# Kernel tuning notes

Hardware: AMD Instinct MI355X
Metric: run time of the kernel (lower is better)

Reference implementation:

```python
import jax, jax.numpy as jnp
import numpy as np

N_NODES = 100000
N_EDGES = 1600000
D_IN = 3      # node_hidden_dim
D_GCN = 128   # gcn_dim


def setup_inputs() -> dict:
    key = jax.random.key(0)
    ks = jax.random.split(key, 10)
    x = jax.random.normal(ks[0], (N_NODES, D_IN), dtype=jnp.float32)
    edge_index = jax.random.randint(ks[1], (2, N_EDGES), 0, N_NODES, dtype=jnp.int64)
    s_in = 1.0 / np.sqrt(D_IN)
    s_h = 1.0 / np.sqrt(D_GCN)
    # PyG SAGEConv: out = lin_l(mean_{j in N(i)} x_j) + lin_r(x_i); bias lives in lin_l
    Wl0 = jax.random.uniform(ks[2], (D_IN, D_GCN), jnp.float32, -s_in, s_in)
    Wr0 = jax.random.uniform(ks[3], (D_IN, D_GCN), jnp.float32, -s_in, s_in)
    b0 = jnp.zeros((D_GCN,), jnp.float32)
    Wl1 = jax.random.uniform(ks[4], (D_GCN, D_GCN), jnp.float32, -s_h, s_h)
    Wr1 = jax.random.uniform(ks[5], (D_GCN, D_GCN), jnp.float32, -s_h, s_h)
    b1 = jnp.zeros((D_GCN,), jnp.float32)
    ln_g = jnp.ones((D_GCN,), jnp.float32)
    ln_b = jnp.zeros((D_GCN,), jnp.float32)
    return {"x": x, "edge_index": edge_index, "Wl0": Wl0, "Wr0": Wr0, "b0": b0,
            "Wl1": Wl1, "Wr1": Wr1, "b1": b1, "ln_g": ln_g, "ln_b": ln_b}


def _sage(h, src, dst, n, inv_deg, Wl, Wr, b):
    # gather source features over edges, mean-reduce onto destinations
    agg = jax.ops.segment_sum(h[src], dst, num_segments=n) * inv_deg  # [N, d]
    return agg @ Wl + h @ Wr + b


def _layernorm(h, g, b, eps=1e-5):
    mu = jnp.mean(h, axis=-1, keepdims=True)
    var = jnp.mean(jnp.square(h - mu), axis=-1, keepdims=True)
    return (h - mu) * jax.lax.rsqrt(var + eps) * g + b


def reference(x, edge_index, Wl0, Wr0, b0, Wl1, Wr1, b1, ln_g, ln_b):
    n = x.shape[0]
    src, dst = edge_index[0], edge_index[1]
    deg = jax.ops.segment_sum(jnp.ones_like(src, dtype=x.dtype), dst, num_segments=n)
    inv_deg = (1.0 / jnp.maximum(deg, 1.0))[:, None]
    h = jax.nn.relu(_sage(x, src, dst, n, inv_deg, Wl0, Wr0, b0))  # dropout = id at eval
    h = _layernorm(h, ln_g, ln_b)
    h = jax.nn.relu(_sage(h, src, dst, n, inv_deg, Wl1, Wr1, b1))
    return h
```

## Files before the change

### kernel.cpp

```cpp
#include <hip/hip_runtime.h>


#define MD 48
#define CAPB 19968
#define MAXBIN 128
#define EPB 4096

#if defined(__has_builtin)
#if __has_builtin(__builtin_amdgcn_cvt_f32_fp8) && __has_builtin(__builtin_amdgcn_cvt_pk_fp8_f32)
#define HAVE_FP8 1
#else
#define HAVE_FP8 0
#endif
#else
#define HAVE_FP8 0
#endif

typedef __attribute__((ext_vector_type(8))) short short8;
typedef __attribute__((ext_vector_type(4))) float floatx4;

__device__ __forceinline__ unsigned bf16_rne(float f) {
    unsigned u = __float_as_uint(f);
    return (u + 0x7FFFu + ((u >> 16) & 1u)) >> 16;
}
__device__ __forceinline__ float bf_lo(unsigned u) { return __uint_as_float(u << 16); }
__device__ __forceinline__ float bf_hi(unsigned u) { return __uint_as_float(u & 0xFFFF0000u); }

__global__ __launch_bounds__(256) void k_binA(
        const int* __restrict__ src, const int* __restrict__ dst,
        int* __restrict__ bcur, unsigned* __restrict__ bins, int E, int nbin) {
    __shared__ int cnt[MAXBIN];
    __shared__ int base[MAXBIN];
    int t = threadIdx.x;
    if (t < MAXBIN) cnt[t] = 0;
    __syncthreads();

    int i0 = blockIdx.x * EPB + t * 16;
    unsigned rec[16];
    int bn[16], rk[16];
    int m = 0;
    if (i0 + 16 <= E) {
#pragma unroll
        for (int q = 0; q < 4; q++) {
            int4 d4 = *(const int4*)&dst[i0 + q * 4];
            int4 s4 = *(const int4*)&src[i0 + q * 4];
            int dd[4] = {d4.x, d4.y, d4.z, d4.w};
            int ss[4] = {s4.x, s4.y, s4.z, s4.w};
#pragma unroll
            for (int j = 0; j < 4; j++) {
                int idx = q * 4 + j;
                bn[idx] = dd[j] >> 10;
                rec[idx] = ((unsigned)(dd[j] & 1023) << 17) | (unsigned)ss[j];
                rk[idx] = atomicAdd(&cnt[bn[idx]], 1);
            }
        }
        m = 16;
    } else {
        for (int j = 0; i0 + j < E && j < 16; j++) {
            int d = dst[i0 + j], s = src[i0 + j];
            bn[j] = d >> 10;
            rec[j] = ((unsigned)(d & 1023) << 17) | (unsigned)s;
            rk[j] = atomicAdd(&cnt[bn[j]], 1);
            m++;
        }
    }
    __syncthreads();
    if (t < nbin) {
        int c = cnt[t];
        base[t] = (c > 0) ? atomicAdd(&bcur[t], c) : 0;
    }
    __syncthreads();
    for (int j = 0; j < m; j++) {
        int g = base[bn[j]] + rk[j];
        if (g < CAPB) bins[(size_t)bn[j] * CAPB + g] = rec[j];
    }
}

__global__ __launch_bounds__(256) void k_binB(
        const unsigned* __restrict__ bins, const int* __restrict__ bcur,
        int* __restrict__ counts, int* __restrict__ slots, int N) {
    __shared__ int cnt[256];
    int t = threadIdx.x;
    int bin = blockIdx.x >> 2, sub = blockIdx.x & 3;
    int llo = sub << 8;
    cnt[t] = 0;
    __syncthreads();
    int total = bcur[bin];
    if (total > CAPB) total = CAPB;
    const unsigned* brow = &bins[(size_t)bin * CAPB];
    int nbase = bin << 10;
    for (int i = t; i < total; i += 1024) {
        unsigned r0 = 0, r1 = 0, r2 = 0, r3 = 0;
        bool h0 = i < total, h1 = i + 256 < total, h2 = i + 512 < total, h3 = i + 768 < total;
        if (h0) r0 = brow[i];
        if (h1) r1 = brow[i + 256];
        if (h2) r2 = brow[i + 512];
        if (h3) r3 = brow[i + 768];
#define DEP(h, rr) if (h) { int dl = (int)(rr >> 17) - llo; \
        if ((unsigned)dl < 256u) { int r = atomicAdd(&cnt[dl], 1); \
            if (r < MD) slots[(size_t)(nbase + llo + dl) * MD + r] = (int)(rr & 0x1FFFFu); } }
        DEP(h0, r0) DEP(h1, r1) DEP(h2, r2) DEP(h3, r3)
#undef DEP
    }
    __syncthreads();
    int node = nbase + llo + t;
    if (node < N) counts[node] = cnt[t];
}

__global__ void k_pack_w(const float* __restrict__ Wl, const float* __restrict__ Wr,
                         uint4* __restrict__ Bp) {
    int g = blockIdx.x * 256 + threadIdx.x;
    int lane = g & 63, jt = (g >> 6) & 7, s = g >> 9;
    int k0 = s * 32 + ((lane >> 4) << 3);
    int n = jt * 16 + (lane & 15);
    unsigned w[4];
#pragma unroll
    for (int p = 0; p < 4; p++) {
        int ka = k0 + 2 * p, kb = k0 + 2 * p + 1;
        float fa = (ka < 128) ? Wl[ka * 128 + n] : Wr[(ka - 128) * 128 + n];
        float fb = (kb < 128) ? Wl[kb * 128 + n] : Wr[(kb - 128) * 128 + n];
        w[p] = bf16_rne(fa) | (bf16_rne(fb) << 16);
    }
    Bp[g] = make_uint4(w[0], w[1], w[2], w[3]);
}

__global__ __launch_bounds__(256) void k_padx(
        const float* __restrict__ x, uint2* __restrict__ xp, int N) {
    int i = blockIdx.x * 256 + threadIdx.x;
    if (i < N) {
        float x0 = x[3 * i], x1 = x[3 * i + 1], x2 = x[3 * i + 2];
        xp[i] = make_uint2(bf16_rne(x0) | (bf16_rne(x1) << 16), bf16_rne(x2));
    }
}

template <int XP>
__global__ __launch_bounds__(256) void k_l0(
        const float* __restrict__ x, const uint2* __restrict__ xp,
        const int* __restrict__ counts, const int* __restrict__ slots,
        const float* __restrict__ Wl0, const float* __restrict__ Wr0,
        const float* __restrict__ b0,
        const float* __restrict__ ln_g, const float* __restrict__ ln_b,
        unsigned* __restrict__ h_bf, unsigned short* __restrict__ h8,
        int use8, int N) {
    __shared__ float sagg[16][8];
    int t = threadIdx.x;
    int grp = t >> 4, sub = t & 15;
    int gnode = blockIdx.x * 16 + grp;
    float a0 = 0, a1 = 0, a2 = 0;
    if (gnode < N) {
        int deg = counts[gnode];
        int dr = min(deg, MD);
        for (int k = sub; k < dr; k += 16) {
            int s = slots[(size_t)gnode * MD + k];
            if (XP) {
                uint2 w = xp[s];
                a0 += bf_lo(w.x);
                a1 += bf_hi(w.x);
                a2 += bf_lo(w.y);
            } else {
                a0 += x[3 * s + 0];
                a1 += x[3 * s + 1];
                a2 += x[3 * s + 2];
            }
        }
#pragma unroll
        for (int off = 8; off; off >>= 1) {
            a0 += __shfl_xor(a0, off, 16);
            a1 += __shfl_xor(a1, off, 16);
            a2 += __shfl_xor(a2, off, 16);
        }
        if (sub == 0) {
            float inv = 1.0f / fmaxf((float)deg, 1.0f);
            sagg[grp][0] = a0 * inv;
            sagg[grp][1] = a1 * inv;
            sagg[grp][2] = a2 * inv;
            sagg[grp][3] = x[3 * gnode + 0];
            sagg[grp][4] = x[3 * gnode + 1];
            sagg[grp][5] = x[3 * gnode + 2];
        }
    }
    __syncthreads();

    int wid = t >> 6, lane = t & 63;
    const float2* Wl = (const float2*)Wl0;
    const float2* Wr = (const float2*)Wr0;
    float2 wl0 = Wl[0 * 64 + lane], wl1 = Wl[1 * 64 + lane], wl2 = Wl[2 * 64 + lane];
    float2 wr0 = Wr[0 * 64 + lane], wr1 = Wr[1 * 64 + lane], wr2 = Wr[2 * 64 + lane];
    float2 bb = ((const float2*)b0)[lane];
    float2 g = ((const float2*)ln_g)[lane];
    float2 lb = ((const float2*)ln_b)[lane];
#pragma unroll
    for (int i = 0; i < 4; i++) {
        int nl = wid * 4 + i;
        int node = blockIdx.x * 16 + nl;
        if (node >= N) break;
        float A0 = sagg[nl][0], A1 = sagg[nl][1], A2 = sagg[nl][2];
        float X0 = sagg[nl][3], X1 = sagg[nl][4], X2 = sagg[nl][5];
        float2 v = bb;
        v.x += A0 * wl0.x + A1 * wl1.x + A2 * wl2.x + X0 * wr0.x + X1 * wr1.x + X2 * wr2.x;
        v.y += A0 * wl0.y + A1 * wl1.y + A2 * wl2.y + X0 * wr0.y + X1 * wr1.y + X2 * wr2.y;
        v.x = fmaxf(v.x, 0.0f); v.y = fmaxf(v.y, 0.0f);
        float s = v.x + v.y, q = v.x * v.x + v.y * v.y;
#pragma unroll
        for (int off = 32; off; off >>= 1) {
            s += __shfl_xor(s, off, 64);
            q += __shfl_xor(q, off, 64);
        }
        float mu = s * (1.0f / 128.0f);
        float var = q * (1.0f / 128.0f) - mu * mu;
        float rstd = rsqrtf(var + 1e-5f);
        float o0 = (v.x - mu) * rstd * g.x + lb.x;
        float o1 = (v.y - mu) * rstd * g.y + lb.y;
        h_bf[(size_t)node * 64 + lane] = bf16_rne(o0) | (bf16_rne(o1) << 16);
#if HAVE_FP8
        if (use8) {
            int p = __builtin_amdgcn_cvt_pk_fp8_f32(o0, o1, 0, false);
            h8[(size_t)node * 64 + lane] = (unsigned short)(p & 0xFFFF);
        }
#endif
    }
}

#define NB 32
#define ROWU 132
template <int U8>
__global__ __launch_bounds__(256) void k_l1f(
        const uint4* __restrict__ Bp, const float* __restrict__ b1,
        const int* __restrict__ counts, const int* __restrict__ slots,
        const unsigned* __restrict__ h_bf, const unsigned short* __restrict__ h8,
        float* __restrict__ out, int N) {
    __shared__ unsigned As[NB * ROWU];
    __shared__ __align__(16) unsigned char stg[4][4096];
    __shared__ int sslot[4][8 * MD];
    int wid = threadIdx.x >> 6, lane = threadIdx.x & 63;
    int nbase = blockIdx.x * NB;

    {
        const int* sp = &slots[(size_t)(nbase + wid * 8) * MD];
#pragma unroll
        for (int u = 0; u < 6; u++) sslot[wid][u * 64 + lane] = sp[u * 64 + lane];
    }

    const int CAP = U8 ? 32 : 16;
    for (int i = 0; i < 8; i++) {
        int nl = wid * 8 + i;
        int node = nbase + nl;
        unsigned aggw = 0, ownw = 0;
        if (node < N) {
            int deg = counts[node];
            int dr = min(deg, MD);
            float inv = 1.0f / fmaxf((float)deg, 1.0f);
            ownw = h_bf[(size_t)node * 64 + lane];
            float a0 = 0.f, a1 = 0.f;
            for (int rb = 0; rb < dr; rb += CAP) {
                int re = min(dr - rb, CAP);
#if HAVE_FP8
                if (U8) {
                    int nin = (re + 7) >> 3;
                    for (int c = 0; c < nin; c++) {
                        int ei = rb + c * 8 + (lane >> 3);
                        int s = (ei < dr) ? (sslot[wid][i * MD + ei] & 0x1FFFF) : 0;
                        const unsigned char* gp = (const unsigned char*)h8
                              + ((size_t)s * 128 + (lane & 7) * 16);
                        __builtin_amdgcn_global_load_lds(
                            (const __attribute__((address_space(1))) unsigned*)gp,
                            (__attribute__((address_space(3))) unsigned*)&stg[wid][c * 1024],
                            16, 0, 0);
                    }
                } else
#endif
                {
                    int nin = (re + 3) >> 2;
                    for (int c = 0; c < nin; c++) {
                        int ei = rb + c * 4 + (lane >> 4);
                        int s = (ei < dr) ? (sslot[wid][i * MD + ei] & 0x1FFFF) : 0;
                        const unsigned char* gp = (const unsigned char*)h_bf
                              + ((size_t)s * 256 + (lane & 15) * 16);
                        __builtin_amdgcn_global_load_lds(
                            (const __attribute__((address_space(1))) unsigned*)gp,
                            (__attribute__((address_space(3))) unsigned*)&stg[wid][c * 1024],
                            16, 0, 0);
                    }
                }
                asm volatile("s_waitcnt vmcnt(0)" ::: "memory");
                __builtin_amdgcn_sched_barrier(0);
#if HAVE_FP8
                if (U8) {
                    const unsigned short* sb = (const unsigned short*)stg[wid];
                    int r = 0;
                    for (; r + 4 <= re; r += 4) {
                        unsigned v0 = sb[(r + 0) * 64 + lane];
                        unsigned v1 = sb[(r + 1) * 64 + lane];
                        unsigned v2 = sb[(r + 2) * 64 + lane];
                        unsigned v3 = sb[(r + 3) * 64 + lane];
                        a0 += (__builtin_amdgcn_cvt_f32_fp8(v0, 0) + __builtin_amdgcn_cvt_f32_fp8(v1, 0))
                            + (__builtin_amdgcn_cvt_f32_fp8(v2, 0) + __builtin_amdgcn_cvt_f32_fp8(v3, 0));
                        a1 += (__builtin_amdgcn_cvt_f32_fp8(v0, 1) + __builtin_amdgcn_cvt_f32_fp8(v1, 1))
                            + (__builtin_amdgcn_cvt_f32_fp8(v2, 1) + __builtin_amdgcn_cvt_f32_fp8(v3, 1));
                    }
                    for (; r < re; r++) {
                        unsigned v = sb[r * 64 + lane];
                        a0 += __builtin_amdgcn_cvt_f32_fp8(v, 0);
                        a1 += __builtin_amdgcn_cvt_f32_fp8(v, 1);
                    }
                } else
#endif
                {
                    const unsigned* sb = (const unsigned*)stg[wid];
                    int r = 0;
                    for (; r + 4 <= re; r += 4) {
                        unsigned v0 = sb[(r + 0) * 64 + lane];
                        unsigned v1 = sb[(r + 1) * 64 + lane];
                        unsigned v2 = sb[(r + 2) * 64 + lane];
                        unsigned v3 = sb[(r + 3) * 64 + lane];
                        a0 += (bf_lo(v0) + bf_lo(v1)) + (bf_lo(v2) + bf_lo(v3));
                        a1 += (bf_hi(v0) + bf_hi(v1)) + (bf_hi(v2) + bf_hi(v3));
                    }
                    for (; r < re; r++) {
                        unsigned v = sb[r * 64 + lane];
                        a0 += bf_lo(v);
                        a1 += bf_hi(v);
                    }
                }
                __builtin_amdgcn_sched_barrier(0);
            }
            aggw = bf16_rne(a0 * inv) | (bf16_rne(a1 * inv) << 16);
        }
        As[nl * ROWU + lane] = aggw;
        As[nl * ROWU + 64 + lane] = ownw;
    }
    __syncthreads();

    int tile = wid >> 1;
    int jh = wid & 1;
    floatx4 acc[4];
#pragma unroll
    for (int jt = 0; jt < 4; jt++) acc[jt] = (floatx4)0.f;
    int arow = tile * 16 + (lane & 15);
    int kq = lane >> 4;
#pragma unroll
    for (int s = 0; s < 8; s++) {
        short8 af = *(const short8*)&As[arow * ROWU + s * 16 + kq * 4];
#pragma unroll
        for (int jt = 0; jt < 4; jt++) {
            short8 bf = ((const short8*)Bp)[(s * 8 + jh * 4 + jt) * 64 + lane];
            acc[jt] = __builtin_amdgcn_mfma_f32_16x16x32_bf16(af, bf, acc[jt], 0, 0, 0);
        }
    }

    int col0 = lane & 15;
#pragma unroll
    for (int r = 0; r < 4; r++) {
        int node = nbase + tile * 16 + (lane >> 4) * 4 + r;
        if (node < N) {
#pragma unroll
            for (int jt = 0; jt < 4; jt++) {
                int col = (jh * 4 + jt) * 16 + col0;
                out[(size_t)node * 128 + col] = fmaxf(acc[jt][r] + b1[col], 0.f);
            }
        }
    }
}

extern "C" void kernel_launch(void* const* d_in, const int* in_sizes, int n_in,
                              void* d_out, int out_size, void* d_ws, size_t ws_size,
                              hipStream_t stream) {
    const float* x    = (const float*)d_in[0];
    const int*   ei   = (const int*)d_in[1];
    const float* Wl0  = (const float*)d_in[2];
    const float* Wr0  = (const float*)d_in[3];
    const float* b0   = (const float*)d_in[4];
    const float* Wl1  = (const float*)d_in[5];
    const float* Wr1  = (const float*)d_in[6];
    const float* b1   = (const float*)d_in[7];
    const float* ln_g = (const float*)d_in[8];
    const float* ln_b = (const float*)d_in[9];
    float* out = (float*)d_out;

    const int N = in_sizes[0] / 3;
    const int E = in_sizes[1] / 2;
    const int* src = ei;
    const int* dst = ei + E;
    const int nbin = (N + 1023) >> 10;

    char* base = (char*)d_ws;
    uint4* Bp            = (uint4*)base;
    int* counts          = (int*)(base + 65536);
    int* bcur            = (int*)(base + 65536 + (size_t)N * 4);
    int* slots           = bcur + MAXBIN;
    char* region         = (char*)(slots + (size_t)N * MD);
    unsigned* bins       = (unsigned*)region;
    unsigned short* h8   = (unsigned short*)region;
    size_t region_off    = 65536 + (size_t)N * 4 + MAXBIN * 4 + (size_t)N * MD * 4;

    int use8 = 0;
#if HAVE_FP8
    if (ws_size >= region_off + (size_t)N * 128 + (size_t)N * 256) use8 = 1;
#endif
    size_t region_sz = use8 ? (size_t)N * 128
                            : (size_t)nbin * CAPB * 4;
    if (region_sz < (size_t)nbin * CAPB * 4) region_sz = (size_t)nbin * CAPB * 4;
    unsigned* h_bf = (unsigned*)(region + region_sz);

    size_t xp_off = region_off + region_sz + (size_t)N * 256;
    int use_xp = (ws_size >= xp_off + (size_t)N * 8) ? 1 : 0;
    uint2* xp = (uint2*)(base + xp_off);

    hipMemsetAsync(counts, 0, (size_t)N * 4 + MAXBIN * 4, stream);
    k_pack_w<<<16, 256, 0, stream>>>(Wl1, Wr1, Bp);
    if (use_xp)
        k_padx<<<(N + 255) / 256, 256, 0, stream>>>(x, xp, N);
    k_binA<<<(E + EPB - 1) / EPB, 256, 0, stream>>>(src, dst, bcur, bins, E, nbin);
    k_binB<<<nbin * 4, 256, 0, stream>>>(bins, bcur, counts, slots, N);
    if (use_xp)
        k_l0<1><<<(N + 15) / 16, 256, 0, stream>>>(x, xp, counts, slots,
                                                   Wl0, Wr0, b0, ln_g, ln_b,
                                                   h_bf, h8, use8, N);
    else
        k_l0<0><<<(N + 15) / 16, 256, 0, stream>>>(x, xp, counts, slots,
                                                   Wl0, Wr0, b0, ln_g, ln_b,
                                                   h_bf, h8, use8, N);
    if (use8)
        k_l1f<1><<<(N + NB - 1) / NB, 256, 0, stream>>>(Bp, b1, counts, slots,
                                                        h_bf, h8, out, N);
    else
        k_l1f<0><<<(N + NB - 1) / NB, 256, 0, stream>>>(Bp, b1, counts, slots,
                                                        h_bf, h8, out, N);
}
```

Before: 235.6 us.

## Replace two-pass binned edge bucketing with direct global-atomic scatter into slots

Drops the two-stage binning (shared-memory bin counts, a global bins buffer, then a per-bin local-atomic scatter) in favour of a single kernel that does a global atomicAdd on counts[dst] and writes src into the fixed-width slot table directly. It also merges the weight-packing and x-padding kernels into one launch. This removes a kernel launch, an intermediate write and read of the bins array, and the workspace region for it. In exchange it issues 1.6M scattered global atomics and writes in random order, which the binning was built to avoid; slot order within a node also becomes nondeterministic.

```diff
diff --git a/kernel.cpp b/kernel.cpp
--- a/kernel.cpp
+++ b/kernel.cpp
@@ -2,9 +2,7 @@
 
 
 #define MD 48
-#define CAPB 19968
-#define MAXBIN 128
-#define EPB 4096
+#define EPT 8
 
 #if defined(__has_builtin)
 #if __has_builtin(__builtin_amdgcn_cvt_f32_fp8) && __has_builtin(__builtin_amdgcn_cvt_pk_fp8_f32)
@@ -26,110 +24,58 @@
 __device__ __forceinline__ float bf_lo(unsigned u) { return __uint_as_float(u << 16); }
 __device__ __forceinline__ float bf_hi(unsigned u) { return __uint_as_float(u & 0xFFFF0000u); }
 
-__global__ __launch_bounds__(256) void k_binA(
+__global__ __launch_bounds__(256) void k_prep(
+        const float* __restrict__ Wl, const float* __restrict__ Wr,
+        uint4* __restrict__ Bp,
+        const float* __restrict__ x, uint2* __restrict__ xp,
+        int N, int use_xp) {
+    int b = blockIdx.x, t = threadIdx.x;
+    if (b < 16) {
+        int g = b * 256 + t;
+        int lane = g & 63, jt = (g >> 6) & 7, s = g >> 9;
+        int k0 = s * 32 + ((lane >> 4) << 3);
+        int n = jt * 16 + (lane & 15);
+        unsigned w[4];
+#pragma unroll
+        for (int p = 0; p < 4; p++) {
+            int ka = k0 + 2 * p, kb = k0 + 2 * p + 1;
+            float fa = (ka < 128) ? Wl[ka * 128 + n] : Wr[(ka - 128) * 128 + n];
+            float fb = (kb < 128) ? Wl[kb * 128 + n] : Wr[(kb - 128) * 128 + n];
+            w[p] = bf16_rne(fa) | (bf16_rne(fb) << 16);
+        }
+        Bp[g] = make_uint4(w[0], w[1], w[2], w[3]);
+    } else if (use_xp) {
+        int i = (b - 16) * 256 + t;
+        if (i < N) {
+            float x0 = x[3 * i], x1 = x[3 * i + 1], x2 = x[3 * i + 2];
+            xp[i] = make_uint2(bf16_rne(x0) | (bf16_rne(x1) << 16), bf16_rne(x2));
+        }
+    }
+}
+
+__global__ __launch_bounds__(256) void k_scatter(
         const int* __restrict__ src, const int* __restrict__ dst,
-        int* __restrict__ bcur, unsigned* __restrict__ bins, int E, int nbin) {
-    __shared__ int cnt[MAXBIN];
-    __shared__ int base[MAXBIN];
-    int t = threadIdx.x;
-    if (t < MAXBIN) cnt[t] = 0;
-    __syncthreads();
-
-    int i0 = blockIdx.x * EPB + t * 16;
-    unsigned rec[16];
-    int bn[16], rk[16];
-    int m = 0;
-    if (i0 + 16 <= E) {
-#pragma unroll
-        for (int q = 0; q < 4; q++) {
+        int* __restrict__ counts, int* __restrict__ slots, int E) {
+    int i0 = (blockIdx.x * 256 + threadIdx.x) * EPT;
+    if (i0 + EPT <= E) {
+#pragma unroll
+        for (int q = 0; q < EPT / 4; q++) {
             int4 d4 = *(const int4*)&dst[i0 + q * 4];
             int4 s4 = *(const int4*)&src[i0 + q * 4];
             int dd[4] = {d4.x, d4.y, d4.z, d4.w};
             int ss[4] = {s4.x, s4.y, s4.z, s4.w};
 #pragma unroll
             for (int j = 0; j < 4; j++) {
-                int idx = q * 4 + j;
-                bn[idx] = dd[j] >> 10;
-                rec[idx] = ((unsigned)(dd[j] & 1023) << 17) | (unsigned)ss[j];
-                rk[idx] = atomicAdd(&cnt[bn[idx]], 1);
+                int r = atomicAdd(&counts[dd[j]], 1);
+                if (r < MD) slots[(size_t)dd[j] * MD + r] = ss[j];
             }
         }
-        m = 16;
     } else {
-        for (int j = 0; i0 + j < E && j < 16; j++) {
+        for (int j = 0; i0 + j < E && j < EPT; j++) {
             int d = dst[i0 + j], s = src[i0 + j];
-            bn[j] = d >> 10;
-            rec[j] = ((unsigned)(d & 1023) << 17) | (unsigned)s;
-            rk[j] = atomicAdd(&cnt[bn[j]], 1);
-            m++;
-        }
-    }
-    __syncthreads();
-    if (t < nbin) {
-        int c = cnt[t];
-        base[t] = (c > 0) ? atomicAdd(&bcur[t], c) : 0;
-    }
-    __syncthreads();
-    for (int j = 0; j < m; j++) {
-        int g = base[bn[j]] + rk[j];
-        if (g < CAPB) bins[(size_t)bn[j] * CAPB + g] = rec[j];
-    }
-}
-
-__global__ __launch_bounds__(256) void k_binB(
-        const unsigned* __restrict__ bins, const int* __restrict__ bcur,
-        int* __restrict__ counts, int* __restrict__ slots, int N) {
-    __shared__ int cnt[256];
-    int t = threadIdx.x;
-    int bin = blockIdx.x >> 2, sub = blockIdx.x & 3;
-    int llo = sub << 8;
-    cnt[t] = 0;
-    __syncthreads();
-    int total = bcur[bin];
-    if (total > CAPB) total = CAPB;
-    const unsigned* brow = &bins[(size_t)bin * CAPB];
-    int nbase = bin << 10;
-    for (int i = t; i < total; i += 1024) {
-        unsigned r0 = 0, r1 = 0, r2 = 0, r3 = 0;
-        bool h0 = i < total, h1 = i + 256 < total, h2 = i + 512 < total, h3 = i + 768 < total;
-        if (h0) r0 = brow[i];
-        if (h1) r1 = brow[i + 256];
-        if (h2) r2 = brow[i + 512];
-        if (h3) r3 = brow[i + 768];
-#define DEP(h, rr) if (h) { int dl = (int)(rr >> 17) - llo; \
-        if ((unsigned)dl < 256u) { int r = atomicAdd(&cnt[dl], 1); \
-            if (r < MD) slots[(size_t)(nbase + llo + dl) * MD + r] = (int)(rr & 0x1FFFFu); } }
-        DEP(h0, r0) DEP(h1, r1) DEP(h2, r2) DEP(h3, r3)
-#undef DEP
-    }
-    __syncthreads();
-    int node = nbase + llo + t;
-    if (node < N) counts[node] = cnt[t];
-}
-
-__global__ void k_pack_w(const float* __restrict__ Wl, const float* __restrict__ Wr,
-                         uint4* __restrict__ Bp) {
-    int g = blockIdx.x * 256 + threadIdx.x;
-    int lane = g & 63, jt = (g >> 6) & 7, s = g >> 9;
-    int k0 = s * 32 + ((lane >> 4) << 3);
-    int n = jt * 16 + (lane & 15);
-    unsigned w[4];
-#pragma unroll
-    for (int p = 0; p < 4; p++) {
-        int ka = k0 + 2 * p, kb = k0 + 2 * p + 1;
-        float fa = (ka < 128) ? Wl[ka * 128 + n] : Wr[(ka - 128) * 128 + n];
-        float fb = (kb < 128) ? Wl[kb * 128 + n] : Wr[(kb - 128) * 128 + n];
-        w[p] = bf16_rne(fa) | (bf16_rne(fb) << 16);
-    }
-    Bp[g] = make_uint4(w[0], w[1], w[2], w[3]);
-}
-
-__global__ __launch_bounds__(256) void k_padx(
-        const float* __restrict__ x, uint2* __restrict__ xp, int N) {
-    int i = blockIdx.x * 256 + threadIdx.x;
-    if (i < N) {
-        float x0 = x[3 * i], x1 = x[3 * i + 1], x2 = x[3 * i + 2];
-        xp[i] = make_uint2(bf16_rne(x0) | (bf16_rne(x1) << 16), bf16_rne(x2));
+            int r = atomicAdd(&counts[d], 1);
+            if (r < MD) slots[(size_t)d * MD + r] = s;
+        }
     }
 }
 
@@ -381,37 +327,28 @@
     const int E = in_sizes[1] / 2;
     const int* src = ei;
     const int* dst = ei + E;
-    const int nbin = (N + 1023) >> 10;
 
     char* base = (char*)d_ws;
     uint4* Bp            = (uint4*)base;
     int* counts          = (int*)(base + 65536);
-    int* bcur            = (int*)(base + 65536 + (size_t)N * 4);
-    int* slots           = bcur + MAXBIN;
-    char* region         = (char*)(slots + (size_t)N * MD);
-    unsigned* bins       = (unsigned*)region;
-    unsigned short* h8   = (unsigned short*)region;
-    size_t region_off    = 65536 + (size_t)N * 4 + MAXBIN * 4 + (size_t)N * MD * 4;
+    int* slots           = counts + N;
+    size_t region_off    = 65536 + (size_t)N * 4 + (size_t)N * MD * 4;
 
     int use8 = 0;
 #if HAVE_FP8
     if (ws_size >= region_off + (size_t)N * 128 + (size_t)N * 256) use8 = 1;
 #endif
-    size_t region_sz = use8 ? (size_t)N * 128
-                            : (size_t)nbin * CAPB * 4;
-    if (region_sz < (size_t)nbin * CAPB * 4) region_sz = (size_t)nbin * CAPB * 4;
-    unsigned* h_bf = (unsigned*)(region + region_sz);
-
-    size_t xp_off = region_off + region_sz + (size_t)N * 256;
+    unsigned short* h8   = (unsigned short*)(base + region_off);
+    unsigned* h_bf       = (unsigned*)(base + region_off + (use8 ? (size_t)N * 128 : 0));
+
+    size_t xp_off = region_off + (use8 ? (size_t)N * 128 : 0) + (size_t)N * 256;
     int use_xp = (ws_size >= xp_off + (size_t)N * 8) ? 1 : 0;
     uint2* xp = (uint2*)(base + xp_off);
 
-    hipMemsetAsync(counts, 0, (size_t)N * 4 + MAXBIN * 4, stream);
-    k_pack_w<<<16, 256, 0, stream>>>(Wl1, Wr1, Bp);
-    if (use_xp)
-        k_padx<<<(N + 255) / 256, 256, 0, stream>>>(x, xp, N);
-    k_binA<<<(E + EPB - 1) / EPB, 256, 0, stream>>>(src, dst, bcur, bins, E, nbin);
-    k_binB<<<nbin * 4, 256, 0, stream>>>(bins, bcur, counts, slots, N);
+    hipMemsetAsync(counts, 0, (size_t)N * 4, stream);
+    k_prep<<<16 + (N + 255) / 256, 256, 0, stream>>>(Wl1, Wr1, Bp, x, xp, N, use_xp);
+    k_scatter<<<(E + 256 * EPT - 1) / (256 * EPT), 256, 0, stream>>>(src, dst,
+                                                                     counts, slots, E);
     if (use_xp)
         k_l0<1><<<(N + 15) / 16, 256, 0, stream>>>(x, xp, counts, slots,
                                                    Wl0, Wr0, b0, ln_g, ln_b,
```

Measured after the change: 306.6 us. +30.1%, slower.
